# Kernel tuning notes

Measured on AMD Instinct MI355X. Metric: run time of the kernel, lower is better.

## Reference

```python
import jax, jax.numpy as jnp
import numpy as np

NUM_HEADS = 32
NUM_KV_HEADS = 8
HEAD_DIM = 128
WINDOW = 512
NUM_META = 4


def _swa_sink_mask(S):
    # allowed = causal & (within sliding window OR sink/meta token)
    i = jnp.arange(S)[:, None]   # q_idx
    j = jnp.arange(S)[None, :]   # kv_idx
    return (i >= j) & (((i - j) <= WINDOW) | (j < NUM_META))


def setup_inputs() -> dict:
    key = jax.random.key(0)
    k1, k2, k3 = jax.random.split(key, 3)
    B, S = 1, 2048
    return {
        "query_states": jax.random.normal(k1, (B, S, NUM_HEADS * HEAD_DIM), dtype=jnp.float32),
        "key_states": jax.random.normal(k2, (B, S, NUM_KV_HEADS * HEAD_DIM), dtype=jnp.float32),
        "value_states": jax.random.normal(k3, (B, S, NUM_KV_HEADS * HEAD_DIM), dtype=jnp.float32),
    }


def reference(query_states, key_states, value_states):
    B, S, _ = query_states.shape
    n_rep = NUM_HEADS // NUM_KV_HEADS
    # [B, H, S, D]
    q = query_states.reshape(B, S, NUM_HEADS, HEAD_DIM).transpose(0, 2, 1, 3)
    k = key_states.reshape(B, S, NUM_KV_HEADS, HEAD_DIM).transpose(0, 2, 1, 3)
    v = value_states.reshape(B, S, NUM_KV_HEADS, HEAD_DIM).transpose(0, 2, 1, 3)
    # repeat_kv: interleaved repeat along head dim (GQA)
    k = jnp.repeat(k, n_rep, axis=1)
    v = jnp.repeat(v, n_rep, axis=1)

    scale = 1.0 / jnp.sqrt(jnp.float32(HEAD_DIM))  # flex_attention default scale
    scores = jnp.einsum("bhqd,bhkd->bhqk", q, k) * scale
    mask = _swa_sink_mask(S)  # [S, S], every row has q_idx==kv_idx allowed
    scores = jnp.where(mask[None, None], scores, -jnp.inf)
    attn = jax.nn.softmax(scores, axis=-1)
    out = jnp.einsum("bhqk,bhkd->bhqd", attn, v)
    return out.transpose(0, 2, 1, 3).reshape(B, S, NUM_HEADS * HEAD_DIM)
```

## Files before the change

### kernel.cpp

```cpp
#include <hip/hip_runtime.h>
#include <math.h>

typedef __attribute__((ext_vector_type(8))) short bf16x8;
typedef __attribute__((ext_vector_type(16))) float f32x16;

#define WIN 512
#define META 4
#define KSTR 132
#define VSTR 68
#define PSTRD 34
#define QSCALE 0.08838834764831845f
#define MFIX 14.0f

union U8 { int4 i4; bf16x8 bf; };

__device__ __forceinline__ unsigned bf16_rne(float x) {
  unsigned u = __float_as_uint(x);
  return (u + 0x7FFFu + ((u >> 16) & 1u)) >> 16;
}
__device__ __forceinline__ unsigned pk2_rne(float a, float b) {
  return bf16_rne(a) | (bf16_rne(b) << 16);
}
__device__ __forceinline__ unsigned pk2_tr(float a, float b) {
  return (__float_as_uint(a) >> 16) | (__float_as_uint(b) & 0xFFFF0000u);
}

__global__ __launch_bounds__(256, 2) void swa_fused(
    const float* __restrict__ Qg, const float* __restrict__ Kg,
    const float* __restrict__ Vg, float* __restrict__ Og)
{
  __shared__ __align__(16) unsigned short Ks[64 * KSTR];
  __shared__ __align__(16) unsigned short Vts[128 * VSTR];
  __shared__ __align__(16) unsigned Pw[4 * 32 * PSTRD];

  const int tid = threadIdx.x;
  const int lane = tid & 63, wid = tid >> 6;
  const int cl = lane & 31, hl = lane >> 5;
  const int hk = blockIdx.y;
  const int h  = hk * 4 + wid;
  const int q0 = blockIdx.x * 32;

  const int sh = tid >> 5;
  const int sc = (tid & 31) * 4;

  int4 qf[8];
  {
    const float* qrow = Qg + (size_t)(q0 + cl) * 4096 + h * 128 + hl * 8;
    #pragma unroll
    for (int kc = 0; kc < 8; ++kc) {
      float4 x = *(const float4*)(qrow + kc * 16);
      float4 y = *(const float4*)(qrow + kc * 16 + 4);
      qf[kc] = make_int4(pk2_rne(x.x*QSCALE, x.y*QSCALE), pk2_rne(x.z*QSCALE, x.w*QSCALE),
                         pk2_rne(y.x*QSCALE, y.y*QSCALE), pk2_rne(y.z*QSCALE, y.w*QSCALE));
    }
  }

  f32x16 acc[4];
  #pragma unroll
  for (int nt = 0; nt < 4; ++nt)
    #pragma unroll
    for (int i = 0; i < 16; ++i) acc[nt][i] = 0.f;
  float lp[16];
  #pragma unroll
  for (int i = 0; i < 16; ++i) lp[i] = 0.f;

  unsigned* PwW = Pw + wid * 32 * PSTRD;

  const int jstart = (q0 > WIN) ? ((q0 - WIN) & ~63) : 0;
  const int sink = (jstart > 0) ? 1 : 0;
  const int niter = ((q0 + 31 - jstart) >> 6) + 1 + sink;

  for (int t = 0; t < niter; ++t) {
    const bool isSink = (sink != 0) && (t == 0);
    const int jt = isSink ? 0 : jstart + ((t - sink) << 6);
    const bool needMask = (jt + 63 > q0) || (q0 + 31 - jt > WIN);

    __syncthreads();

    #pragma unroll
    for (int it = 0; it < 8; ++it) {
      const int row = it * 8 + sh;
      float4 v = *(const float4*)(Kg + (size_t)(jt + row) * 1024 + hk * 128 + sc);
      *(uint2*)(Ks + row * KSTR + sc) = make_uint2(pk2_tr(v.x, v.y), pk2_tr(v.z, v.w));
    }
    {
      float4 vv[8];
      #pragma unroll
      for (int it = 0; it < 8; ++it)
        vv[it] = *(const float4*)(Vg + (size_t)(jt + it * 8 + sh) * 1024 + hk * 128 + sc);
      #pragma unroll
      for (int i2 = 0; i2 < 4; ++i2) {
        const int key = i2 * 8 + sh;
        const int woff = 2 * (key & 3);
        const int gb = key >> 2;
        const float lo[4] = {vv[i2].x, vv[i2].y, vv[i2].z, vv[i2].w};
        const float hi[4] = {vv[i2+4].x, vv[i2+4].y, vv[i2+4].z, vv[i2+4].w};
        #pragma unroll
        for (int j = 0; j < 4; ++j) {
          const int d = sc + j;
          Vts[0] += 0;
          *(unsigned*)(&Vts[d * VSTR + ((gb ^ (d & 7)) << 3) + woff]) = pk2_tr(lo[j], hi[j]);
        }
      }
    }
    __syncthreads();

    f32x16 s0v, s1v;
    #pragma unroll
    for (int i = 0; i < 16; ++i) { s0v[i] = 0.f; s1v[i] = 0.f; }
    #pragma unroll
    for (int kc = 0; kc < 8; ++kc) {
      U8 a; a.i4 = qf[kc];
      const unsigned short* k0p = Ks + cl * KSTR + kc * 16 + hl * 8;
      U8 b0; { uint2 lo = *(const uint2*)k0p; uint2 hi = *(const uint2*)(k0p + 4);
               b0.i4 = make_int4(lo.x, lo.y, hi.x, hi.y); }
      s0v = __builtin_amdgcn_mfma_f32_32x32x16_bf16(a.bf, b0.bf, s0v, 0, 0, 0);
      const unsigned short* k1p = k0p + 32 * KSTR;
      U8 b1; { uint2 lo = *(const uint2*)k1p; uint2 hi = *(const uint2*)(k1p + 4);
               b1.i4 = make_int4(lo.x, lo.y, hi.x, hi.y); }
      s1v = __builtin_amdgcn_mfma_f32_32x32x16_bf16(a.bf, b1.bf, s1v, 0, 0, 0);
    }

    const int k0 = jt + cl, k1 = jt + 32 + cl;
    #pragma unroll
    for (int ri = 0; ri < 16; ++ri) {
      const int rl = (ri & 3) + 8 * (ri >> 2) + 4 * hl;
      float sa = s0v[ri] - MFIX;
      float sb = s1v[ri] - MFIX;
      if (needMask) {
        const int row = q0 + rl;
        const int d0 = row - k0, d1 = row - k1;
        if (!((d0 >= 0) && ((d0 <= WIN) || (k0 < META)))) sa = -1e30f;
        if (!((d1 >= 0) && ((d1 <= WIN) || (k1 < META)))) sb = -1e30f;
      }
      float p0 = __expf(sa), p1 = __expf(sb);
      unsigned u0 = __float_as_uint(p0) & 0xFFFF0000u;
      unsigned u1 = __float_as_uint(p1) & 0xFFFF0000u;
      lp[ri] += __uint_as_float(u0) + __uint_as_float(u1);
      PwW[rl * PSTRD + cl] = (u0 >> 16) | u1;
    }

    const int kcmax = isSink ? 1 : 4;
    for (int kc = 0; kc < kcmax; ++kc) {
      const unsigned* ap = PwW + cl * PSTRD + kc * 8 + hl * 4;
      U8 a; { uint2 lo = *(const uint2*)ap; uint2 hi = *(const uint2*)(ap + 2);
              a.i4 = make_int4(lo.x, lo.y, hi.x, hi.y); }
      const int g = ((kc * 2 + hl) ^ (cl & 7)) << 3;
      #pragma unroll
      for (int nt = 0; nt < 4; ++nt) {
        const unsigned short* vp = Vts + (nt * 32 + cl) * VSTR + g;
        U8 b; { uint2 lo = *(const uint2*)vp; uint2 hi = *(const uint2*)(vp + 4);
                b.i4 = make_int4(lo.x, lo.y, hi.x, hi.y); }
        acc[nt] = __builtin_amdgcn_mfma_f32_32x32x16_bf16(a.bf, b.bf, acc[nt], 0, 0, 0);
      }
    }
  }

  #pragma unroll
  for (int ri = 0; ri < 16; ++ri) {
    float v = lp[ri];
    v += __shfl_xor(v, 1);  v += __shfl_xor(v, 2);  v += __shfl_xor(v, 4);
    v += __shfl_xor(v, 8);  v += __shfl_xor(v, 16);
    lp[ri] = __fdividef(1.0f, v);
  }
  #pragma unroll
  for (int nt = 0; nt < 4; ++nt) {
    #pragma unroll
    for (int ri = 0; ri < 16; ++ri) {
      const int rl = (ri & 3) + 8 * (ri >> 2) + 4 * hl;
      Og[(size_t)(q0 + rl) * 4096 + h * 128 + nt * 32 + cl] = acc[nt][ri] * lp[ri];
    }
  }
}

extern "C" void kernel_launch(void* const* d_in, const int* in_sizes, int n_in,
                              void* d_out, int out_size, void* d_ws, size_t ws_size,
                              hipStream_t stream) {
  const float* Q = (const float*)d_in[0];
  const float* K = (const float*)d_in[1];
  const float* V = (const float*)d_in[2];
  float* O = (float*)d_out;
  hipLaunchKernelGGL(swa_fused, dim3(64, 8), dim3(256), 0, stream, Q, K, V, O);
}
```

Before: 136.0 us.

## Prefetch next K/V tile into registers, widen LDS reads, balance tile order

Loads the next K/V tile from global memory into registers right after the barrier, so those loads overlap with the current tile's MFMA work instead of stalling before the LDS store. Changes the LDS strides and the V transpose/swizzle layout so every operand read is a single 16-byte LDS load instead of two 8-byte loads. Interleaves query tiles from the start and end of the sequence across block indices to balance causal work. Costs extra registers for the prefetch buffers, which may lower occupancy under the 2-blocks-per-SM launch bound.

```diff
diff --git a/kernel.cpp b/kernel.cpp
--- a/kernel.cpp
+++ b/kernel.cpp
@@ -6,9 +6,9 @@
 
 #define WIN 512
 #define META 4
-#define KSTR 132
-#define VSTR 68
-#define PSTRD 34
+#define KSTR 136
+#define VSTR 72
+#define PSTRD 36
 #define QSCALE 0.08838834764831845f
 #define MFIX 14.0f
 
@@ -38,10 +38,15 @@
   const int cl = lane & 31, hl = lane >> 5;
   const int hk = blockIdx.y;
   const int h  = hk * 4 + wid;
-  const int q0 = blockIdx.x * 32;
+  const int bx = blockIdx.x;
+  const int qtile = (bx & 1) ? (63 - (bx >> 1)) : (bx >> 1);
+  const int q0 = qtile * 32;
 
   const int sh = tid >> 5;
   const int sc = (tid & 31) * 4;
+  const int kq = tid >> 4;
+  const int dg = tid & 15;
+  const int vchi = ((kq >> 1) ^ (dg & 7)) * 8 + (kq & 1) * 4;
 
   int4 qf[8];
   {
@@ -70,6 +75,22 @@
   const int sink = (jstart > 0) ? 1 : 0;
   const int niter = ((q0 + 31 - jstart) >> 6) + 1 + sink;
 
+  float4 kreg[8], vreg[8];
+  {
+    const int jt0 = sink ? 0 : jstart;
+    const float* kb = Kg + (size_t)jt0 * 1024 + hk * 128 + sc;
+    #pragma unroll
+    for (int it = 0; it < 8; ++it)
+      kreg[it] = *(const float4*)(kb + (size_t)(it * 8 + sh) * 1024);
+    const float* vb = Vg + (size_t)jt0 * 1024 + hk * 128 + dg * 8;
+    #pragma unroll
+    for (int r = 0; r < 4; ++r) {
+      const int row = ((r & 1) ? 1 : 0) + ((r >> 1) ? 32 : 0) + 2 * kq;
+      vreg[2*r]   = *(const float4*)(vb + (size_t)row * 1024);
+      vreg[2*r+1] = *(const float4*)(vb + (size_t)row * 1024 + 4);
+    }
+  }
+
   for (int t = 0; t < niter; ++t) {
     const bool isSink = (sink != 0) && (t == 0);
     const int jt = isSink ? 0 : jstart + ((t - sink) << 6);
@@ -79,31 +100,39 @@
 
     #pragma unroll
     for (int it = 0; it < 8; ++it) {
-      const int row = it * 8 + sh;
-      float4 v = *(const float4*)(Kg + (size_t)(jt + row) * 1024 + hk * 128 + sc);
-      *(uint2*)(Ks + row * KSTR + sc) = make_uint2(pk2_tr(v.x, v.y), pk2_tr(v.z, v.w));
-    }
-    {
-      float4 vv[8];
+      float4 v = kreg[it];
+      *(uint2*)(Ks + (it * 8 + sh) * KSTR + sc) =
+          make_uint2(pk2_tr(v.x, v.y), pk2_tr(v.z, v.w));
+    }
+    #pragma unroll
+    for (int half = 0; half < 2; ++half) {
+      const float* p0 = (const float*)&vreg[half];
+      const float* p1 = (const float*)&vreg[2 + half];
+      const float* p2 = (const float*)&vreg[4 + half];
+      const float* p3 = (const float*)&vreg[6 + half];
+      #pragma unroll
+      for (int e = 0; e < 4; ++e) {
+        const int dp = dg * 8 + half * 4 + e;
+        *(uint2*)(Vts + dp * VSTR + vchi) =
+            make_uint2(pk2_tr(p0[e], p2[e]), pk2_tr(p1[e], p3[e]));
+      }
+    }
+    __syncthreads();
+
+    if (t + 1 < niter) {
+      const int jn = jstart + ((t + 1 - sink) << 6);
+      const float* kb = Kg + (size_t)jn * 1024 + hk * 128 + sc;
       #pragma unroll
       for (int it = 0; it < 8; ++it)
-        vv[it] = *(const float4*)(Vg + (size_t)(jt + it * 8 + sh) * 1024 + hk * 128 + sc);
-      #pragma unroll
-      for (int i2 = 0; i2 < 4; ++i2) {
-        const int key = i2 * 8 + sh;
-        const int woff = 2 * (key & 3);
-        const int gb = key >> 2;
-        const float lo[4] = {vv[i2].x, vv[i2].y, vv[i2].z, vv[i2].w};
-        const float hi[4] = {vv[i2+4].x, vv[i2+4].y, vv[i2+4].z, vv[i2+4].w};
-        #pragma unroll
-        for (int j = 0; j < 4; ++j) {
-          const int d = sc + j;
-          Vts[0] += 0;
-          *(unsigned*)(&Vts[d * VSTR + ((gb ^ (d & 7)) << 3) + woff]) = pk2_tr(lo[j], hi[j]);
-        }
-      }
-    }
-    __syncthreads();
+        kreg[it] = *(const float4*)(kb + (size_t)(it * 8 + sh) * 1024);
+      const float* vb = Vg + (size_t)jn * 1024 + hk * 128 + dg * 8;
+      #pragma unroll
+      for (int r = 0; r < 4; ++r) {
+        const int row = ((r & 1) ? 1 : 0) + ((r >> 1) ? 32 : 0) + 2 * kq;
+        vreg[2*r]   = *(const float4*)(vb + (size_t)row * 1024);
+        vreg[2*r+1] = *(const float4*)(vb + (size_t)row * 1024 + 4);
+      }
+    }
 
     f32x16 s0v, s1v;
     #pragma unroll
@@ -111,13 +140,9 @@
     #pragma unroll
     for (int kc = 0; kc < 8; ++kc) {
       U8 a; a.i4 = qf[kc];
-      const unsigned short* k0p = Ks + cl * KSTR + kc * 16 + hl * 8;
-      U8 b0; { uint2 lo = *(const uint2*)k0p; uint2 hi = *(const uint2*)(k0p + 4);
-               b0.i4 = make_int4(lo.x, lo.y, hi.x, hi.y); }
+      U8 b0; b0.i4 = *(const int4*)(Ks + cl * KSTR + kc * 16 + hl * 8);
       s0v = __builtin_amdgcn_mfma_f32_32x32x16_bf16(a.bf, b0.bf, s0v, 0, 0, 0);
-      const unsigned short* k1p = k0p + 32 * KSTR;
-      U8 b1; { uint2 lo = *(const uint2*)k1p; uint2 hi = *(const uint2*)(k1p + 4);
-               b1.i4 = make_int4(lo.x, lo.y, hi.x, hi.y); }
+      U8 b1; b1.i4 = *(const int4*)(Ks + (32 + cl) * KSTR + kc * 16 + hl * 8);
       s1v = __builtin_amdgcn_mfma_f32_32x32x16_bf16(a.bf, b1.bf, s1v, 0, 0, 0);
     }
 
@@ -142,15 +167,12 @@
 
     const int kcmax = isSink ? 1 : 4;
     for (int kc = 0; kc < kcmax; ++kc) {
-      const unsigned* ap = PwW + cl * PSTRD + kc * 8 + hl * 4;
-      U8 a; { uint2 lo = *(const uint2*)ap; uint2 hi = *(const uint2*)(ap + 2);
-              a.i4 = make_int4(lo.x, lo.y, hi.x, hi.y); }
-      const int g = ((kc * 2 + hl) ^ (cl & 7)) << 3;
+      U8 a; a.i4 = *(const int4*)(PwW + cl * PSTRD + kc * 8 + hl * 4);
       #pragma unroll
       for (int nt = 0; nt < 4; ++nt) {
-        const unsigned short* vp = Vts + (nt * 32 + cl) * VSTR + g;
-        U8 b; { uint2 lo = *(const uint2*)vp; uint2 hi = *(const uint2*)(vp + 4);
-                b.i4 = make_int4(lo.x, lo.y, hi.x, hi.y); }
+        const int dim = nt * 32 + cl;
+        const int chi = ((2 * kc + hl) ^ ((dim >> 3) & 7)) * 8;
+        U8 b; b.i4 = *(const int4*)(Vts + dim * VSTR + chi);
         acc[nt] = __builtin_amdgcn_mfma_f32_32x32x16_bf16(a.bf, b.bf, acc[nt], 0, 0, 0);
       }
     }
```

After: 132.9 us. -2.3%, faster.
